# Optimization experiments

Hardware: AMD Instinct MI355X
Metric: run time of the kernel (lower is better)

## Reference

```python
import jax, jax.numpy as jnp
import numpy as np

B, N, D = 4, 4096, 2048
H = 16          # heads
KH = 16         # k_per_head (must equal heads for the view to be valid)
DK = D // H     # 128


def setup_inputs() -> dict:
    key = jax.random.key(0)
    kx, kq, kk, kv, ko = jax.random.split(key, 5)
    s = 1.0 / np.sqrt(D).astype(np.float32)  # ~torch Linear init scale
    return {
        "x": jax.random.normal(kx, (B, N, D), jnp.float32),
        "Wq": jax.random.normal(kq, (D, D), jnp.float32) * s,
        "Wk": jax.random.normal(kk, (D, D), jnp.float32) * s,
        "Wv": jax.random.normal(kv, (D, D), jnp.float32) * s,
        "Wo": jax.random.normal(ko, (D, D), jnp.float32) * s,
    }


def reference(x, Wq, Wk, Wv, Wo):
    b, n, d = x.shape
    # QKV projections (bias-free Linear; weight stored as (in, out))
    q = (x @ Wq).reshape(b, n, H, DK)    # (B,N,H,DK)
    k = (x @ Wk).reshape(b, n, KH, DK)   # (B,N,KH,DK)
    v = (x @ Wv).reshape(b, n, KH, DK)   # (B,N,KH,DK)
    # softmax-free matmul chain, batched per token: (H,DK)@(DK,KH)@(KH,DK)
    scores = jnp.einsum("bnhd,bnkd->bnhk", q, k)   # (B,N,H,KH)
    o = jnp.einsum("bnhk,bnkd->bnhd", scores, v)   # (B,N,H,DK)
    return o.reshape(b, n, d) @ Wo                 # (B,N,D)
```

## Files before the change

kernel.cpp:

```cpp
#include <hip/hip_runtime.h>
#include <hip/hip_bf16.h>

#define BB 4
#define NN 4096
#define DD 2048
#define HH 16
#define DK 128
#define MTOK (BB * NN)
#define QKVW (3 * DD)

typedef __bf16 bf16x8 __attribute__((ext_vector_type(8)));
typedef __bf16 bf16x4 __attribute__((ext_vector_type(4)));
typedef float f32x4 __attribute__((ext_vector_type(4)));
typedef float f32x16 __attribute__((ext_vector_type(16)));

__device__ __forceinline__ void gload16(const __bf16* g, __bf16* lds_wave_uniform_base) {
    __builtin_amdgcn_global_load_lds(
        (const __attribute__((address_space(1))) void*)g,
        (__attribute__((address_space(3))) void*)lds_wave_uniform_base,
        16, 0, 0);
}

__global__ __launch_bounds__(256) void xconv_kernel(const float* __restrict__ X,
                                                    __bf16* __restrict__ Xb, int n4) {
    int i = blockIdx.x * blockDim.x + threadIdx.x;
    if (i < n4) {
        float4 v = reinterpret_cast<const float4*>(X)[i];
        bf16x4 o;
        o[0] = (__bf16)v.x; o[1] = (__bf16)v.y; o[2] = (__bf16)v.z; o[3] = (__bf16)v.w;
        reinterpret_cast<bf16x4*>(Xb)[i] = o;
    }
}

__global__ __launch_bounds__(256) void wconv_kernel(const float* __restrict__ W0,
                                                    const float* __restrict__ W1,
                                                    const float* __restrict__ W2,
                                                    const float* __restrict__ W3,
                                                    __bf16* __restrict__ Wcat,
                                                    __bf16* __restrict__ Wo_t) {
    __shared__ float tile[32][33];
    const int w = blockIdx.z;
    const float* W = (w == 0) ? W0 : (w == 1) ? W1 : (w == 2) ? W2 : W3;
    __bf16* dst = (w < 3) ? (Wcat + (size_t)w * DD * DD) : Wo_t;
    const int tx = threadIdx.x, ty = threadIdx.y;
    const int n0 = blockIdx.x * 32, k0 = blockIdx.y * 32;
#pragma unroll
    for (int j = 0; j < 32; j += 8)
        tile[ty + j][tx] = W[(size_t)(k0 + ty + j) * DD + n0 + tx];
    __syncthreads();
#pragma unroll
    for (int j = 0; j < 32; j += 8)
        dst[(size_t)(n0 + ty + j) * DD + k0 + tx] = (__bf16)tile[tx][ty + j];
}

template <typename OutT>
__global__ __launch_bounds__(256) void gemm_bt(const __bf16* __restrict__ A, int lda,
                                               const __bf16* __restrict__ Bt, int ldb,
                                               OutT* __restrict__ C, int ldc, int K) {
    constexpr int BM = 128, BN = 128, BK = 64;
    __shared__ __align__(16) __bf16 As[BM * BK];
    __shared__ __align__(16) __bf16 Bs[BN * BK];

    const int tid = threadIdx.x;
    const int wave = tid >> 6;
    const int lane = tid & 63;
    const int m32 = lane & 31;
    const int half = lane >> 5;
    const int wm = wave >> 1;
    const int wn = wave & 1;
    const size_t blockM = blockIdx.y * BM;
    const size_t blockN = blockIdx.x * BN;

    const int srow = lane >> 3;
    const int scol = ((lane & 7) ^ srow) * 8;

    f32x16 acc[2][2] = {};

    for (int k0 = 0; k0 < K; k0 += BK) {
#pragma unroll
        for (int it = 0; it < 4; ++it) {
            const int rbase = it * 32 + wave * 8;
            const int r = rbase + srow;
            gload16(A + (blockM + r) * (size_t)lda + k0 + scol, &As[rbase * BK]);
            gload16(Bt + (blockN + r) * (size_t)ldb + k0 + scol, &Bs[rbase * BK]);
        }
        __syncthreads();

#pragma unroll
        for (int ks = 0; ks < 4; ++ks) {
            const int chunk = ((ks * 2 + half) ^ (m32 & 7)) * 8;
            bf16x8 af[2], bfr[2];
#pragma unroll
            for (int mi = 0; mi < 2; ++mi)
                af[mi] = *reinterpret_cast<const bf16x8*>(
                    As + (wm * 64 + mi * 32 + m32) * BK + chunk);
#pragma unroll
            for (int ni = 0; ni < 2; ++ni)
                bfr[ni] = *reinterpret_cast<const bf16x8*>(
                    Bs + (wn * 64 + ni * 32 + m32) * BK + chunk);
#pragma unroll
            for (int mi = 0; mi < 2; ++mi)
#pragma unroll
                for (int ni = 0; ni < 2; ++ni)
                    acc[mi][ni] = __builtin_amdgcn_mfma_f32_32x32x16_bf16(
                        af[mi], bfr[ni], acc[mi][ni], 0, 0, 0);
        }
        __syncthreads();
    }

#pragma unroll
    for (int mi = 0; mi < 2; ++mi) {
#pragma unroll
        for (int ni = 0; ni < 2; ++ni) {
            const size_t col = blockN + wn * 64 + ni * 32 + m32;
#pragma unroll
            for (int reg = 0; reg < 16; ++reg) {
                const size_t row = blockM + wm * 64 + mi * 32 +
                                   (reg & 3) + 8 * (reg >> 2) + 4 * half;
                C[row * (size_t)ldc + col] = (OutT)acc[mi][ni][reg];
            }
        }
    }
}

__global__ __launch_bounds__(256) void attn_kernel(const __bf16* __restrict__ qkv,
                                                   __bf16* __restrict__ Ob) {
    __shared__ float sc[4][16][17];
    const int tid = threadIdx.x;
    const int wave = tid >> 6;
    const int lane = tid & 63;
    const int t = lane & 15;
    const int quad = lane >> 4;
    const size_t token = (size_t)blockIdx.x * 4 + wave;
    const __bf16* row = qkv + token * QKVW;
    __bf16* orow = Ob + token * DD;

    f32x4 s = (f32x4){0.f, 0.f, 0.f, 0.f};
#pragma unroll
    for (int ks = 0; ks < 4; ++ks) {
        bf16x8 a = *reinterpret_cast<const bf16x8*>(row + t * DK + ks * 32 + quad * 8);
        bf16x8 b = *reinterpret_cast<const bf16x8*>(row + DD + t * DK + ks * 32 + quad * 8);
        s = __builtin_amdgcn_mfma_f32_16x16x32_bf16(a, b, s, 0, 0, 0);
    }
#pragma unroll
    for (int i = 0; i < 4; ++i) sc[wave][quad * 4 + i][t] = s[i];
    __syncthreads();

    const int d0 = t * 8;
    float oa[4][8];
#pragma unroll
    for (int i = 0; i < 4; ++i)
#pragma unroll
        for (int e = 0; e < 8; ++e) oa[i][e] = 0.f;

#pragma unroll
    for (int j = 0; j < 16; ++j) {
        bf16x8 v8 = *reinterpret_cast<const bf16x8*>(row + 2 * DD + j * DK + d0);
        float vf[8];
#pragma unroll
        for (int e = 0; e < 8; ++e) vf[e] = (float)v8[e];
#pragma unroll
        for (int i = 0; i < 4; ++i) {
            const float sj = sc[wave][quad + 4 * i][j];
#pragma unroll
            for (int e = 0; e < 8; ++e) oa[i][e] += sj * vf[e];
        }
    }
#pragma unroll
    for (int i = 0; i < 4; ++i) {
        bf16x8 o8;
#pragma unroll
        for (int e = 0; e < 8; ++e) o8[e] = (__bf16)oa[i][e];
        *reinterpret_cast<bf16x8*>(orow + (quad + 4 * i) * DK + d0) = o8;
    }
}

extern "C" void kernel_launch(void* const* d_in, const int* in_sizes, int n_in,
                              void* d_out, int out_size, void* d_ws, size_t ws_size,
                              hipStream_t stream) {
    const float* X  = (const float*)d_in[0];
    const float* Wq = (const float*)d_in[1];
    const float* Wk = (const float*)d_in[2];
    const float* Wv = (const float*)d_in[3];
    const float* Wo = (const float*)d_in[4];
    float* out = (float*)d_out;

    char* ws = (char*)d_ws;
    __bf16* Wcat = (__bf16*)ws;
    __bf16* Wo_t = (__bf16*)(ws + (size_t)3 * DD * DD * 2);
    __bf16* Xb   = (__bf16*)(ws + (size_t)4 * DD * DD * 2);
    __bf16* QKV  = (__bf16*)(ws + (size_t)4 * DD * DD * 2 + (size_t)MTOK * DD * 2);
    __bf16* Ob   = Xb;

    const int n4 = MTOK * DD / 4;
    xconv_kernel<<<(n4 + 255) / 256, 256, 0, stream>>>(X, Xb, n4);

    wconv_kernel<<<dim3(DD / 32, DD / 32, 4), dim3(32, 8), 0, stream>>>(
        Wq, Wk, Wv, Wo, Wcat, Wo_t);

    gemm_bt<__bf16><<<dim3(QKVW / 128, MTOK / 128), 256, 0, stream>>>(
        Xb, DD, Wcat, DD, QKV, QKVW, DD);

    attn_kernel<<<MTOK / 4, 256, 0, stream>>>(QKV, Ob);

    gemm_bt<float><<<dim3(DD / 128, MTOK / 128), 256, 0, stream>>>(
        Ob, DD, Wo_t, DD, out, DD, DD);
}
```

Baseline: 901.6 us.

## Replace GEMM with 256x256 double-buffered pipelined MFMA kernel

Replaces the 128x128 single-buffered GEMM with a 256x256-tile, 512-thread kernel. It double-buffers LDS, interleaves global-to-LDS loads for the next k-tile with MFMA phases, uses 16x16x32 MFMAs, raises wave priority around compute, and remaps workgroups in a swizzled order for cache locality. The aim is to hide global load latency and raise arithmetic intensity in both projection GEMMs. In exchange it uses more registers and LDS, and relies on hand-placed waitcnt and barrier ordering that could be fragile.

```diff
diff --git a/kernel.cpp b/kernel.cpp
--- a/kernel.cpp
+++ b/kernel.cpp
@@ -12,7 +12,6 @@
 typedef __bf16 bf16x8 __attribute__((ext_vector_type(8)));
 typedef __bf16 bf16x4 __attribute__((ext_vector_type(4)));
 typedef float f32x4 __attribute__((ext_vector_type(4)));
-typedef float f32x16 __attribute__((ext_vector_type(16)));
 
 __device__ __forceinline__ void gload16(const __bf16* g, __bf16* lds_wave_uniform_base) {
     __builtin_amdgcn_global_load_lds(
@@ -54,71 +53,168 @@
 }
 
 template <typename OutT>
-__global__ __launch_bounds__(256) void gemm_bt(const __bf16* __restrict__ A, int lda,
-                                               const __bf16* __restrict__ Bt, int ldb,
-                                               OutT* __restrict__ C, int ldc, int K) {
-    constexpr int BM = 128, BN = 128, BK = 64;
-    __shared__ __align__(16) __bf16 As[BM * BK];
-    __shared__ __align__(16) __bf16 Bs[BN * BK];
+__global__ __launch_bounds__(512, 2) void gemm256(const __bf16* __restrict__ A, int lda,
+                                                  const __bf16* __restrict__ Bt, int ldb,
+                                                  OutT* __restrict__ C, int ldc, int K) {
+    __shared__ __align__(16) __bf16 lds[2][4][8192];
+    const int NT = K >> 6;
 
     const int tid = threadIdx.x;
-    const int wave = tid >> 6;
-    const int lane = tid & 63;
-    const int m32 = lane & 31;
-    const int half = lane >> 5;
-    const int wm = wave >> 1;
-    const int wn = wave & 1;
-    const size_t blockM = blockIdx.y * BM;
-    const size_t blockN = blockIdx.x * BN;
-
-    const int srow = lane >> 3;
-    const int scol = ((lane & 7) ^ srow) * 8;
-
-    f32x16 acc[2][2] = {};
-
-    for (int k0 = 0; k0 < K; k0 += BK) {
-#pragma unroll
-        for (int it = 0; it < 4; ++it) {
-            const int rbase = it * 32 + wave * 8;
-            const int r = rbase + srow;
-            gload16(A + (blockM + r) * (size_t)lda + k0 + scol, &As[rbase * BK]);
-            gload16(Bt + (blockN + r) * (size_t)ldb + k0 + scol, &Bs[rbase * BK]);
-        }
-        __syncthreads();
-
-#pragma unroll
-        for (int ks = 0; ks < 4; ++ks) {
-            const int chunk = ((ks * 2 + half) ^ (m32 & 7)) * 8;
-            bf16x8 af[2], bfr[2];
-#pragma unroll
-            for (int mi = 0; mi < 2; ++mi)
-                af[mi] = *reinterpret_cast<const bf16x8*>(
-                    As + (wm * 64 + mi * 32 + m32) * BK + chunk);
-#pragma unroll
-            for (int ni = 0; ni < 2; ++ni)
-                bfr[ni] = *reinterpret_cast<const bf16x8*>(
-                    Bs + (wn * 64 + ni * 32 + m32) * BK + chunk);
-#pragma unroll
-            for (int mi = 0; mi < 2; ++mi)
-#pragma unroll
-                for (int ni = 0; ni < 2; ++ni)
-                    acc[mi][ni] = __builtin_amdgcn_mfma_f32_32x32x16_bf16(
-                        af[mi], bfr[ni], acc[mi][ni], 0, 0, 0);
-        }
-        __syncthreads();
-    }
-
-#pragma unroll
-    for (int mi = 0; mi < 2; ++mi) {
-#pragma unroll
-        for (int ni = 0; ni < 2; ++ni) {
-            const size_t col = blockN + wn * 64 + ni * 32 + m32;
-#pragma unroll
-            for (int reg = 0; reg < 16; ++reg) {
-                const size_t row = blockM + wm * 64 + mi * 32 +
-                                   (reg & 3) + 8 * (reg >> 2) + 4 * half;
-                C[row * (size_t)ldc + col] = (OutT)acc[mi][ni][reg];
-            }
+    const int wave = tid >> 6, lane = tid & 63;
+    const int wm = wave >> 2, wn = wave & 3;
+
+    const int nbx = gridDim.x;
+    const int nwg = nbx * gridDim.y;
+    int flat = blockIdx.y * nbx + blockIdx.x;
+    flat = (flat & 7) * (nwg >> 3) + (flat >> 3);
+    const size_t blockM = (size_t)(flat / nbx) * 256;
+    const size_t blockN = (size_t)(flat % nbx) * 256;
+
+    const int kel = ((((lane >> 1) ^ (lane >> 5)) & 1) << 4) + ((lane & 1) << 3);
+    const __bf16* sA = A + (blockM + (size_t)(lane >> 2)) * lda + kel;
+    const __bf16* sB = Bt + (blockN + (size_t)(lane >> 2)) * ldb + kel;
+
+    const int ldsOff = (lane & 15) * 64 + (((lane >> 4) * 16) ^ (((lane >> 3) & 1) << 5));
+    const int aOff = wm * 8192 + ldsOff;
+    const int bOff = wn * 4096 + ldsOff;
+
+#define STAGE_A(t, khc)                                                                   \
+    do {                                                                                  \
+        const int _k = (t) * 64 + (khc) * 32;                                             \
+        gload16(sA + (size_t)(wave * 32) * lda + _k,                                      \
+                &lds[(t) & 1][(khc)][wave * 1024]);                                       \
+        gload16(sA + (size_t)(wave * 32 + 16) * lda + _k,                                 \
+                &lds[(t) & 1][(khc)][wave * 1024 + 512]);                                 \
+    } while (0)
+#define STAGE_B(t, khc)                                                                   \
+    do {                                                                                  \
+        const int _k = (t) * 64 + (khc) * 32;                                             \
+        gload16(sB + (size_t)(wave * 32) * ldb + _k,                                      \
+                &lds[(t) & 1][2 + (khc)][wave * 1024]);                                   \
+        gload16(sB + (size_t)(wave * 32 + 16) * ldb + _k,                                 \
+                &lds[(t) & 1][2 + (khc)][wave * 1024 + 512]);                             \
+    } while (0)
+
+    f32x4 acc[8][4] = {};
+
+    STAGE_A(0, 0); STAGE_B(0, 0); STAGE_A(0, 1); STAGE_B(0, 1);
+    STAGE_A(1, 0);
+    asm volatile("s_waitcnt vmcnt(2)" ::: "memory");
+    asm volatile("s_barrier" ::: "memory");
+
+#pragma unroll 2
+    for (int T = 0; T < NT; ++T) {
+        const int b = T & 1;
+        bf16x8 bk0[4], bk1[4];
+
+        {
+            bf16x8 af[4];
+            const char* Ag = (const char*)&lds[b][0][0];
+            const char* Bg = (const char*)&lds[b][2][0];
+#pragma unroll
+            for (int mi = 0; mi < 4; ++mi)
+                af[mi] = *(const bf16x8*)(Ag + aOff + mi * 1024);
+#pragma unroll
+            for (int ni = 0; ni < 4; ++ni)
+                bk0[ni] = *(const bf16x8*)(Bg + bOff + ni * 1024);
+            if (T + 1 < NT) STAGE_B(T + 1, 0);
+            asm volatile("s_barrier" ::: "memory");
+            __builtin_amdgcn_sched_barrier(0);
+            __builtin_amdgcn_s_setprio(1);
+#pragma unroll
+            for (int mi = 0; mi < 4; ++mi)
+#pragma unroll
+                for (int ni = 0; ni < 4; ++ni)
+                    acc[mi][ni] = __builtin_amdgcn_mfma_f32_16x16x32_bf16(
+                        af[mi], bk0[ni], acc[mi][ni], 0, 0, 0);
+            __builtin_amdgcn_sched_barrier(0);
+            __builtin_amdgcn_s_setprio(0);
+            asm volatile("s_barrier" ::: "memory");
+        }
+
+        {
+            bf16x8 af[4];
+            const char* Ag = (const char*)&lds[b][1][0];
+            const char* Bg = (const char*)&lds[b][3][0];
+#pragma unroll
+            for (int mi = 0; mi < 4; ++mi)
+                af[mi] = *(const bf16x8*)(Ag + aOff + mi * 1024);
+#pragma unroll
+            for (int ni = 0; ni < 4; ++ni)
+                bk1[ni] = *(const bf16x8*)(Bg + bOff + ni * 1024);
+            if (T + 1 < NT) STAGE_A(T + 1, 1);
+            asm volatile("s_barrier" ::: "memory");
+            __builtin_amdgcn_sched_barrier(0);
+            __builtin_amdgcn_s_setprio(1);
+#pragma unroll
+            for (int mi = 0; mi < 4; ++mi)
+#pragma unroll
+                for (int ni = 0; ni < 4; ++ni)
+                    acc[mi][ni] = __builtin_amdgcn_mfma_f32_16x16x32_bf16(
+                        af[mi], bk1[ni], acc[mi][ni], 0, 0, 0);
+            __builtin_amdgcn_sched_barrier(0);
+            __builtin_amdgcn_s_setprio(0);
+            asm volatile("s_barrier" ::: "memory");
+        }
+
+        {
+            bf16x8 af[4];
+            const char* Ag = (const char*)&lds[b][0][0];
+#pragma unroll
+            for (int mi = 0; mi < 4; ++mi)
+                af[mi] = *(const bf16x8*)(Ag + aOff + 4096 + mi * 1024);
+            if (T + 1 < NT) STAGE_B(T + 1, 1);
+            asm volatile("s_barrier" ::: "memory");
+            __builtin_amdgcn_sched_barrier(0);
+            __builtin_amdgcn_s_setprio(1);
+#pragma unroll
+            for (int mi = 0; mi < 4; ++mi)
+#pragma unroll
+                for (int ni = 0; ni < 4; ++ni)
+                    acc[4 + mi][ni] = __builtin_amdgcn_mfma_f32_16x16x32_bf16(
+                        af[mi], bk0[ni], acc[4 + mi][ni], 0, 0, 0);
+            __builtin_amdgcn_sched_barrier(0);
+            __builtin_amdgcn_s_setprio(0);
+            asm volatile("s_barrier" ::: "memory");
+        }
+
+        {
+            bf16x8 af[4];
+            const char* Ag = (const char*)&lds[b][1][0];
+#pragma unroll
+            for (int mi = 0; mi < 4; ++mi)
+                af[mi] = *(const bf16x8*)(Ag + aOff + 4096 + mi * 1024);
+            if (T + 2 < NT) STAGE_A(T + 2, 0);
+            asm volatile("s_barrier" ::: "memory");
+            __builtin_amdgcn_sched_barrier(0);
+            __builtin_amdgcn_s_setprio(1);
+#pragma unroll
+            for (int mi = 0; mi < 4; ++mi)
+#pragma unroll
+                for (int ni = 0; ni < 4; ++ni)
+                    acc[4 + mi][ni] = __builtin_amdgcn_mfma_f32_16x16x32_bf16(
+                        af[mi], bk1[ni], acc[4 + mi][ni], 0, 0, 0);
+            __builtin_amdgcn_sched_barrier(0);
+            __builtin_amdgcn_s_setprio(0);
+            if (T + 2 < NT) asm volatile("s_waitcnt vmcnt(2)" ::: "memory");
+            else            asm volatile("s_waitcnt vmcnt(0)" ::: "memory");
+            asm volatile("s_barrier" ::: "memory");
+        }
+    }
+#undef STAGE_A
+#undef STAGE_B
+
+    const int rEp = (lane >> 4) * 4;
+    const int cEp = lane & 15;
+#pragma unroll
+    for (int mi = 0; mi < 8; ++mi) {
+        const size_t row0 = blockM + wm * 128 + mi * 16 + rEp;
+#pragma unroll
+        for (int ni = 0; ni < 4; ++ni) {
+            const size_t col = blockN + wn * 64 + ni * 16 + cEp;
+#pragma unroll
+            for (int r = 0; r < 4; ++r)
+                C[(row0 + r) * (size_t)ldc + col] = (OutT)acc[mi][ni][r];
         }
     }
 }
@@ -198,11 +294,11 @@
     wconv_kernel<<<dim3(DD / 32, DD / 32, 4), dim3(32, 8), 0, stream>>>(
         Wq, Wk, Wv, Wo, Wcat, Wo_t);
 
-    gemm_bt<__bf16><<<dim3(QKVW / 128, MTOK / 128), 256, 0, stream>>>(
+    gemm256<__bf16><<<dim3(QKVW / 256, MTOK / 256), 512, 0, stream>>>(
         Xb, DD, Wcat, DD, QKV, QKVW, DD);
 
     attn_kernel<<<MTOK / 4, 256, 0, stream>>>(QKV, Ob);
 
-    gemm_bt<float><<<dim3(DD / 128, MTOK / 128), 256, 0, stream>>>(
+    gemm256<float><<<dim3(DD / 256, MTOK / 256), 512, 0, stream>>>(
         Ob, DD, Wo_t, DD, out, DD, DD);
 }
```

After: 819.0 us. 9.2% less time.
